# Performance work log

Measured on AMD Instinct MI355X. Metric: run time of the kernel, lower is better.

## Reference

```python
import jax, jax.numpy as jnp
import numpy as np

B, N, K = 4, 50000, 128   # batch, surface points, deformation nodes
GD = 128                  # SDF grid resolution (D=H=W)


def setup_inputs() -> dict:
    key = jax.random.key(0)
    ks = jax.random.split(key, 7)
    constants = jax.random.normal(ks[0], (B, K), dtype=jnp.float32)
    scales = 0.05 + 0.25 * jax.random.uniform(ks[1], (B, K), dtype=jnp.float32)
    # proper-ish rotations via QR of random matrices
    M = jax.random.normal(ks[2], (B, K, 3, 3), dtype=jnp.float32)
    rotations, _ = jnp.linalg.qr(M)
    centers = jax.random.uniform(ks[3], (B, K, 3), dtype=jnp.float32, minval=-0.5, maxval=0.5)
    surface_samples = jax.random.uniform(ks[4], (B, N, 6), dtype=jnp.float32, minval=-0.5, maxval=0.5)
    grid = jax.random.normal(ks[5], (B, GD, GD, GD), dtype=jnp.float32)
    # world2grid maps world [-0.5,0.5] -> grid index [0, GD-1]
    w2g = np.zeros((B, 4, 4), dtype=np.float32)
    w2g[:, 0, 0] = w2g[:, 1, 1] = w2g[:, 2, 2] = float(GD - 1)
    w2g[:, :3, 3] = float(GD - 1) / 2.0
    w2g[:, 3, 3] = 1.0
    world2grid = jnp.asarray(w2g)
    return {"constants": constants, "scales": scales, "rotations": rotations,
            "centers": centers, "surface_samples": surface_samples,
            "grid": grid, "world2grid": world2grid}


def _trilinear_border(vol, xyz):
    """torch grid_sample (5D, bilinear, align_corners=True, border) for one batch.
    vol: (D,H,W); xyz: (N,3) normalized coords in [-1,1], order (x,y,z)."""
    D, H, W = vol.shape
    x = jnp.clip((xyz[:, 0] + 1.0) * 0.5 * (W - 1), 0.0, W - 1)
    y = jnp.clip((xyz[:, 1] + 1.0) * 0.5 * (H - 1), 0.0, H - 1)
    z = jnp.clip((xyz[:, 2] + 1.0) * 0.5 * (D - 1), 0.0, D - 1)
    x0 = jnp.floor(x); y0 = jnp.floor(y); z0 = jnp.floor(z)
    fx = x - x0; fy = y - y0; fz = z - z0
    x0i = x0.astype(jnp.int32); x1i = jnp.minimum(x0i + 1, W - 1)
    y0i = y0.astype(jnp.int32); y1i = jnp.minimum(y0i + 1, H - 1)
    z0i = z0.astype(jnp.int32); z1i = jnp.minimum(z0i + 1, D - 1)
    c000 = vol[z0i, y0i, x0i]; c001 = vol[z0i, y0i, x1i]
    c010 = vol[z0i, y1i, x0i]; c011 = vol[z0i, y1i, x1i]
    c100 = vol[z1i, y0i, x0i]; c101 = vol[z1i, y0i, x1i]
    c110 = vol[z1i, y1i, x0i]; c111 = vol[z1i, y1i, x1i]
    c00 = c000 * (1 - fx) + c001 * fx
    c01 = c010 * (1 - fx) + c011 * fx
    c10 = c100 * (1 - fx) + c101 * fx
    c11 = c110 * (1 - fx) + c111 * fx
    c0 = c00 * (1 - fy) + c01 * fy
    c1 = c10 * (1 - fy) + c11 * fy
    return c0 * (1 - fz) + c1 * fz


def reference(constants, scales, rotations, centers, surface_samples, grid, world2grid):
    pts = surface_samples[..., :3]                       # (B,N,3)
    diff = pts[:, :, None, :] - centers[:, None, :, :]   # (B,N,K,3)  == p - t_source
    d2 = jnp.sum(diff * diff, axis=-1)                   # (B,N,K)
    # sample_rbf_weights with use_constants=True
    w = jnp.exp(-d2 / (2.0 * scales * scales)[:, None, :]) * (constants * constants)[:, None, :]
    w = w / jnp.sum(w, axis=-1, keepdims=True)           # normalize over nodes

    # target = roll batch by -1 (source_idx+1 mod B)
    R_t = jnp.roll(rotations, -1, axis=0)
    R_rel = jnp.einsum('bkij,bklj->bkil', R_t, rotations)       # R_target @ R_source^T
    c_t = jnp.roll(centers, -1, axis=0)
    transformed = jnp.einsum('bkij,bnkj->bnki', R_rel, diff) + c_t[:, None, :, :]
    blended = jnp.einsum('bnk,bnki->bni', w, transformed)        # (B,N,3)

    w2g_t = jnp.roll(world2grid, -1, axis=0)
    A = w2g_t[:, :3, :3]
    t = w2g_t[:, :3, 3]
    gcs = jnp.einsum('bij,bnj->bni', A, blended) + t[:, None, :]  # grid coords (x,y,z)

    D, H, W = grid.shape[1], grid.shape[2], grid.shape[3]
    denom = jnp.array([W - 1, H - 1, D - 1], dtype=gcs.dtype)
    gcs = 2.0 * (gcs / denom) - 1.0                               # normalize to [-1,1]

    grid_t = jnp.roll(grid, -1, axis=0)
    sdf = jax.vmap(_trilinear_border)(grid_t, gcs)                # (B,N)
    return jnp.sum(jnp.mean(sdf * sdf, axis=1))
```

## Files before the change

### kernel.cpp

```cpp
#include <hip/hip_runtime.h>
#include <stdint.h>

#define K_   128
#define GD_  128
#define PSTR 20
#define KPW  32

static __device__ __forceinline__ float fast_exp2(float x) {
#if __has_builtin(__builtin_amdgcn_exp2f)
    return __builtin_amdgcn_exp2f(x);
#else
    return exp2f(x);
#endif
}

__global__ void surf_param_kernel(
    const float* __restrict__ constants,
    const float* __restrict__ scales,
    const float* __restrict__ rotations,
    const float* __restrict__ centers,
    const float* __restrict__ w2g,
    float* __restrict__ params,
    float* __restrict__ out,
    int B)
{
    int idx = blockIdx.x * blockDim.x + threadIdx.x;
    if (idx == 0) out[0] = 0.0f;
    if (idx >= B * K_) return;
    int b = idx / K_, k = idx - b * K_;
    int bn = (b + 1 == B) ? 0 : (b + 1);
    const float L2E = 1.4426950408889634f;

    const float* R  = rotations + (size_t)(b  * K_ + k) * 9;
    const float* Rt = rotations + (size_t)(bn * K_ + k) * 9;
    float m[9];
#pragma unroll
    for (int i = 0; i < 3; ++i)
#pragma unroll
        for (int l = 0; l < 3; ++l)
            m[i * 3 + l] = Rt[i * 3 + 0] * R[l * 3 + 0]
                         + Rt[i * 3 + 1] * R[l * 3 + 1]
                         + Rt[i * 3 + 2] * R[l * 3 + 2];

    const float* Aw = w2g + (size_t)bn * 16;
    float G[9], A[9] = {Aw[0], Aw[1], Aw[2], Aw[4], Aw[5], Aw[6], Aw[8], Aw[9], Aw[10]};
    float T[3] = {Aw[3], Aw[7], Aw[11]};
#pragma unroll
    for (int i = 0; i < 3; ++i)
#pragma unroll
        for (int l = 0; l < 3; ++l)
            G[i * 3 + l] = A[i * 3 + 0] * m[0 * 3 + l]
                         + A[i * 3 + 1] * m[1 * 3 + l]
                         + A[i * 3 + 2] * m[2 * 3 + l];

    const float* c  = centers + (size_t)(b  * K_ + k) * 3;
    const float* ct = centers + (size_t)(bn * K_ + k) * 3;
    float c0 = c[0], c1 = c[1], c2 = c[2];
    float vw0 = ct[0] - (m[0] * c0 + m[1] * c1 + m[2] * c2);
    float vw1 = ct[1] - (m[3] * c0 + m[4] * c1 + m[5] * c2);
    float vw2 = ct[2] - (m[6] * c0 + m[7] * c1 + m[8] * c2);
    float v0 = A[0] * vw0 + A[1] * vw1 + A[2] * vw2 + T[0];
    float v1 = A[3] * vw0 + A[4] * vw1 + A[5] * vw2 + T[1];
    float v2 = A[6] * vw0 + A[7] * vw1 + A[8] * vw2 + T[2];

    float sig = scales[b * K_ + k];
    float s   = 1.0f / (2.0f * sig * sig);
    float con = constants[b * K_ + k];
    float s2n = -s * L2E;
    float r   = log2f(con * con) + s2n * (c0 * c0 + c1 * c1 + c2 * c2);

    float* o = params + (size_t)idx * PSTR;
    o[0] = G[0]; o[1] = G[1]; o[2] = G[2]; o[3] = G[3];
    o[4] = G[4]; o[5] = G[5]; o[6] = G[6]; o[7] = G[7];
    o[8] = G[8]; o[9] = v0;  o[10] = v1;  o[11] = v2;
    o[12] = -2.0f * s2n * c0;
    o[13] = -2.0f * s2n * c1;
    o[14] = -2.0f * s2n * c2;
    o[15] = r;
    o[16] = s2n;
    o[17] = 0.f; o[18] = 0.f; o[19] = 0.f;
}

__global__ __launch_bounds__(256) void surf_loss_kernel(
    const float* __restrict__ sp,
    const float* __restrict__ grid,
    const float* __restrict__ params,
    float* __restrict__ out,
    int N, int B, int bpb)
{
    __shared__ float  lds_par[K_ * PSTR];
    __shared__ float4 lds_part[4 * 4 * 64];
    __shared__ float  red[4];

    const int tid  = threadIdx.x;
    const int lane = tid & 63;
    const int wave = tid >> 6;
    const int blk  = blockIdx.x;
    const int b    = blk / bpb;
    const int base = (blk - b * bpb) * 256;
    const int bn   = (b + 1 == B) ? 0 : (b + 1);

    {
        const float4* Pv = (const float4*)(params + (size_t)b * K_ * PSTR);
        float4* Lv = (float4*)lds_par;
        for (int t = tid; t < K_ * PSTR / 4; t += 256)
            Lv[t] = Pv[t];
    }

    float px[4], py[4], pz[4], pq[4];
    float ax[4], ay[4], az[4], aw[4];
    const float* spb = sp + (size_t)b * N * 6;
#pragma unroll
    for (int j = 0; j < 4; ++j) {
        int n = base + j * 64 + lane;
        int nn = (n < N) ? n : 0;
        const float* q = spb + (size_t)nn * 6;
        px[j] = q[0]; py[j] = q[1]; pz[j] = q[2];
        pq[j] = px[j] * px[j] + py[j] * py[j] + pz[j] * pz[j];
        ax[j] = 0.f; ay[j] = 0.f; az[j] = 0.f; aw[j] = 0.f;
    }

    __syncthreads();

    const int k0 = wave * KPW;
#pragma unroll 2
    for (int kk = 0; kk < KPW; ++kk) {
        const float4* f = (const float4*)(lds_par + (k0 + kk) * PSTR);
        const float4 f0 = f[0];
        const float4 f1 = f[1];
        const float4 f2 = f[2];
        const float4 f3 = f[3];
        const float  s2 = lds_par[(k0 + kk) * PSTR + 16];
#pragma unroll
        for (int j = 0; j < 4; ++j) {
            float e = f3.w + f3.x * px[j] + f3.y * py[j] + f3.z * pz[j] + s2 * pq[j];
            float w = fast_exp2(e);
            float tx = f2.y + f0.x * px[j] + f0.y * py[j] + f0.z * pz[j];
            float ty = f2.z + f0.w * px[j] + f1.x * py[j] + f1.y * pz[j];
            float tz = f2.w + f1.z * px[j] + f1.w * py[j] + f2.x * pz[j];
            ax[j] += w * tx;
            ay[j] += w * ty;
            az[j] += w * tz;
            aw[j] += w;
        }
    }

#pragma unroll
    for (int j = 0; j < 4; ++j)
        lds_part[((wave * 4 + j) << 6) + lane] = make_float4(ax[j], ay[j], az[j], aw[j]);
    __syncthreads();

    float accum = 0.0f;
    {
        int n = base + wave * 64 + lane;
        if (n < N) {
            float sx = 0.f, sy = 0.f, sz = 0.f, sw = 0.f;
#pragma unroll
            for (int w = 0; w < 4; ++w) {
                float4 t = lds_part[((w * 4 + wave) << 6) + lane];
                sx += t.x; sy += t.y; sz += t.z; sw += t.w;
            }
            float inv = 1.0f / sw;
            float x = fminf(fmaxf(sx * inv, 0.0f), (float)(GD_ - 1));
            float y = fminf(fmaxf(sy * inv, 0.0f), (float)(GD_ - 1));
            float z = fminf(fmaxf(sz * inv, 0.0f), (float)(GD_ - 1));
            float x0f = floorf(x), y0f = floorf(y), z0f = floorf(z);
            float fx = x - x0f, fy = y - y0f, fz = z - z0f;
            int x0 = (int)x0f, y0 = (int)y0f, z0 = (int)z0f;
            int x1 = x0 + 1 > GD_ - 1 ? GD_ - 1 : x0 + 1;
            int y1 = y0 + 1 > GD_ - 1 ? GD_ - 1 : y0 + 1;
            int z1 = z0 + 1 > GD_ - 1 ? GD_ - 1 : z0 + 1;
            const float* gb = grid + (size_t)bn * GD_ * GD_ * GD_;
            int zy00 = (z0 * GD_ + y0) * GD_;
            int zy01 = (z0 * GD_ + y1) * GD_;
            int zy10 = (z1 * GD_ + y0) * GD_;
            int zy11 = (z1 * GD_ + y1) * GD_;
            float c000 = gb[zy00 + x0], c001 = gb[zy00 + x1];
            float c010 = gb[zy01 + x0], c011 = gb[zy01 + x1];
            float c100 = gb[zy10 + x0], c101 = gb[zy10 + x1];
            float c110 = gb[zy11 + x0], c111 = gb[zy11 + x1];
            float ofx = 1.0f - fx, ofy = 1.0f - fy, ofz = 1.0f - fz;
            float c00 = c000 * ofx + c001 * fx;
            float c01 = c010 * ofx + c011 * fx;
            float c10 = c100 * ofx + c101 * fx;
            float c11 = c110 * ofx + c111 * fx;
            float c0 = c00 * ofy + c01 * fy;
            float c1 = c10 * ofy + c11 * fy;
            float sdf = c0 * ofz + c1 * fz;
            accum = sdf * sdf;
        }
    }

#pragma unroll
    for (int off = 32; off > 0; off >>= 1)
        accum += __shfl_down(accum, off, 64);
    if (lane == 0) red[wave] = accum;
    __syncthreads();
    if (tid == 0)
        atomicAdd(out, (red[0] + red[1] + red[2] + red[3]) * (1.0f / (float)N));
}

extern "C" void kernel_launch(void* const* d_in, const int* in_sizes, int n_in,
                              void* d_out, int out_size, void* d_ws, size_t ws_size,
                              hipStream_t stream) {
    const float* constants = (const float*)d_in[0];
    const float* scales    = (const float*)d_in[1];
    const float* rotations = (const float*)d_in[2];
    const float* centers   = (const float*)d_in[3];
    const float* sp        = (const float*)d_in[4];
    const float* grid      = (const float*)d_in[5];
    const float* w2g       = (const float*)d_in[6];
    float* out = (float*)d_out;
    float* params = (float*)d_ws;

    const int B = in_sizes[6] / 16;
    const int N = in_sizes[4] / (6 * B);

    int np = B * K_;
    hipLaunchKernelGGL(surf_param_kernel, dim3((np + 255) / 256), dim3(256), 0, stream,
                       constants, scales, rotations, centers, w2g, params, out, B);

    const int bpb = (N + 255) / 256;
    hipLaunchKernelGGL(surf_loss_kernel, dim3(B * bpb), dim3(256), 0, stream,
                       sp, grid, params, out, N, B, bpb);
}
```

Before: 113.1 us.

## Double points per thread and read node params directly from global memory

Each thread now handles 8 points instead of 4, so a block covers 512 points, and the grid shrinks to half as many blocks. The per-block staging of node parameters into LDS and its barrier are removed. Each wave instead reads its 32 nodes' parameters straight from global memory as wave-uniform loads. The loads are thought to land in scalar or L1 cache, and reuse per load doubles. The cost is more registers, capped by a launch bound of 2 blocks, and fewer blocks to fill the GPU (about 392).

```diff
diff --git a/kernel.cpp b/kernel.cpp
--- a/kernel.cpp
+++ b/kernel.cpp
@@ -5,6 +5,8 @@
 #define GD_  128
 #define PSTR 20
 #define KPW  32
+#define J_   8
+#define PPB  (64 * J_)
 
 static __device__ __forceinline__ float fast_exp2(float x) {
 #if __has_builtin(__builtin_amdgcn_exp2f)
@@ -81,15 +83,14 @@
     o[17] = 0.f; o[18] = 0.f; o[19] = 0.f;
 }
 
-__global__ __launch_bounds__(256) void surf_loss_kernel(
+__global__ __launch_bounds__(256, 2) void surf_loss_kernel(
     const float* __restrict__ sp,
     const float* __restrict__ grid,
     const float* __restrict__ params,
     float* __restrict__ out,
     int N, int B, int bpb)
 {
-    __shared__ float  lds_par[K_ * PSTR];
-    __shared__ float4 lds_part[4 * 4 * 64];
+    __shared__ float4 lds_part[4 * J_ * 64];
     __shared__ float  red[4];
 
     const int tid  = threadIdx.x;
@@ -97,22 +98,15 @@
     const int wave = tid >> 6;
     const int blk  = blockIdx.x;
     const int b    = blk / bpb;
-    const int base = (blk - b * bpb) * 256;
+    const int base = (blk - b * bpb) * PPB;
     const int bn   = (b + 1 == B) ? 0 : (b + 1);
 
-    {
-        const float4* Pv = (const float4*)(params + (size_t)b * K_ * PSTR);
-        float4* Lv = (float4*)lds_par;
-        for (int t = tid; t < K_ * PSTR / 4; t += 256)
-            Lv[t] = Pv[t];
-    }
-
-    float px[4], py[4], pz[4], pq[4];
-    float ax[4], ay[4], az[4], aw[4];
+    float px[J_], py[J_], pz[J_], pq[J_];
+    float ax[J_], ay[J_], az[J_], aw[J_];
     const float* spb = sp + (size_t)b * N * 6;
 #pragma unroll
-    for (int j = 0; j < 4; ++j) {
-        int n = base + j * 64 + lane;
+    for (int j = 0; j < J_; ++j) {
+        int n = base + (j << 6) + lane;
         int nn = (n < N) ? n : 0;
         const float* q = spb + (size_t)nn * 6;
         px[j] = q[0]; py[j] = q[1]; pz[j] = q[2];
@@ -120,19 +114,17 @@
         ax[j] = 0.f; ay[j] = 0.f; az[j] = 0.f; aw[j] = 0.f;
     }
 
-    __syncthreads();
-
-    const int k0 = wave * KPW;
+    const float4* Pv = (const float4*)(params
+                     + ((size_t)b * K_ + (size_t)wave * KPW) * PSTR);
 #pragma unroll 2
     for (int kk = 0; kk < KPW; ++kk) {
-        const float4* f = (const float4*)(lds_par + (k0 + kk) * PSTR);
-        const float4 f0 = f[0];
-        const float4 f1 = f[1];
-        const float4 f2 = f[2];
-        const float4 f3 = f[3];
-        const float  s2 = lds_par[(k0 + kk) * PSTR + 16];
-#pragma unroll
-        for (int j = 0; j < 4; ++j) {
+        const float4 f0 = Pv[kk * 5 + 0];
+        const float4 f1 = Pv[kk * 5 + 1];
+        const float4 f2 = Pv[kk * 5 + 2];
+        const float4 f3 = Pv[kk * 5 + 3];
+        const float  s2 = Pv[kk * 5 + 4].x;
+#pragma unroll
+        for (int j = 0; j < J_; ++j) {
             float e = f3.w + f3.x * px[j] + f3.y * py[j] + f3.z * pz[j] + s2 * pq[j];
             float w = fast_exp2(e);
             float tx = f2.y + f0.x * px[j] + f0.y * py[j] + f0.z * pz[j];
@@ -146,20 +138,24 @@
     }
 
 #pragma unroll
-    for (int j = 0; j < 4; ++j)
-        lds_part[((wave * 4 + j) << 6) + lane] = make_float4(ax[j], ay[j], az[j], aw[j]);
+    for (int j = 0; j < J_; ++j)
+        lds_part[((wave * J_ + j) << 6) + lane] = make_float4(ax[j], ay[j], az[j], aw[j]);
     __syncthreads();
 
     float accum = 0.0f;
-    {
-        int n = base + wave * 64 + lane;
+    const float* gb = grid + (size_t)bn * GD_ * GD_ * GD_;
+#pragma unroll
+    for (int e2 = 0; e2 < 2; ++e2) {
+        int pi = (e2 << 8) + tid;
+        int j  = pi >> 6, ln = pi & 63;
+        float sx = 0.f, sy = 0.f, sz = 0.f, sw = 0.f;
+#pragma unroll
+        for (int w = 0; w < 4; ++w) {
+            float4 t = lds_part[((w * J_ + j) << 6) + ln];
+            sx += t.x; sy += t.y; sz += t.z; sw += t.w;
+        }
+        int n = base + pi;
         if (n < N) {
-            float sx = 0.f, sy = 0.f, sz = 0.f, sw = 0.f;
-#pragma unroll
-            for (int w = 0; w < 4; ++w) {
-                float4 t = lds_part[((w * 4 + wave) << 6) + lane];
-                sx += t.x; sy += t.y; sz += t.z; sw += t.w;
-            }
             float inv = 1.0f / sw;
             float x = fminf(fmaxf(sx * inv, 0.0f), (float)(GD_ - 1));
             float y = fminf(fmaxf(sy * inv, 0.0f), (float)(GD_ - 1));
@@ -170,7 +166,6 @@
             int x1 = x0 + 1 > GD_ - 1 ? GD_ - 1 : x0 + 1;
             int y1 = y0 + 1 > GD_ - 1 ? GD_ - 1 : y0 + 1;
             int z1 = z0 + 1 > GD_ - 1 ? GD_ - 1 : z0 + 1;
-            const float* gb = grid + (size_t)bn * GD_ * GD_ * GD_;
             int zy00 = (z0 * GD_ + y0) * GD_;
             int zy01 = (z0 * GD_ + y1) * GD_;
             int zy10 = (z1 * GD_ + y0) * GD_;
@@ -187,7 +182,7 @@
             float c0 = c00 * ofy + c01 * fy;
             float c1 = c10 * ofy + c11 * fy;
             float sdf = c0 * ofz + c1 * fz;
-            accum = sdf * sdf;
+            accum += sdf * sdf;
         }
     }
 
@@ -220,7 +215,7 @@
     hipLaunchKernelGGL(surf_param_kernel, dim3((np + 255) / 256), dim3(256), 0, stream,
                        constants, scales, rotations, centers, w2g, params, out, B);
 
-    const int bpb = (N + 255) / 256;
+    const int bpb = (N + PPB - 1) / PPB;
     hipLaunchKernelGGL(surf_loss_kernel, dim3(B * bpb), dim3(256), 0, stream,
                        sp, grid, params, out, N, B, bpb);
 }
```

New measurement: 118.7 us. 1.05x slower.
